# Optimization experiments

Measured on AMD Instinct MI355X. Metric: run time of the kernel, lower is better.

## Reference

```python
import jax, jax.numpy as jnp
import numpy as np

NUM_HEADS = 16
EMBED_DIM = 2048
MAX_SEQ = 2048
HEAD_SIZE = EMBED_DIM // NUM_HEADS  # 128
ROPE_BASE = 10000.0


def setup_inputs() -> dict:
    key = jax.random.key(0)
    k1, k2, k3 = jax.random.split(key, 3)
    B, S = 4, 2048
    x = jax.random.normal(k1, (B, S, EMBED_DIM), dtype=jnp.float32)
    positions = jnp.arange(S, dtype=jnp.int32)
    # causal boolean mask: query i may attend to key j iff j <= i
    mask = jnp.tril(jnp.ones((S, MAX_SEQ), dtype=bool))[None, None]
    Wqkv = jax.random.normal(k2, (EMBED_DIM, 3 * EMBED_DIM), dtype=jnp.float32) * 0.02
    Wout = jax.random.normal(k3, (EMBED_DIM, EMBED_DIM), dtype=jnp.float32) * 0.02
    return {"x": x, "positions": positions, "mask": mask, "Wqkv": Wqkv, "Wout": Wout}


def _rope(x, positions):
    # x: [B, S, H, hd]; rotate interleaved (even, odd) pairs in last dim
    inv_freq = 1.0 / (ROPE_BASE ** (jnp.arange(0, HEAD_SIZE, 2, dtype=jnp.float32) / HEAD_SIZE))
    freq = positions.astype(jnp.float32)[:, None] * inv_freq[None, :]  # [S, hd/2]
    cos = jnp.cos(freq)[None, :, None, :]  # [1, S, 1, hd/2]
    sin = jnp.sin(freq)[None, :, None, :]
    xp = x.reshape(*x.shape[:-1], HEAD_SIZE // 2, 2)
    x0, x1 = xp[..., 0], xp[..., 1]
    out = jnp.stack([x0 * cos - x1 * sin, x1 * cos + x0 * sin], axis=-1)
    return out.reshape(x.shape)


def reference(x, positions, mask, Wqkv, Wout):
    B, S, D = x.shape
    H, hd = NUM_HEADS, HEAD_SIZE
    qkv = x @ Wqkv  # [B, S, 3D]
    q, k, v = jnp.split(qkv, 3, axis=-1)
    q = q.reshape(B, S, H, hd)
    k = k.reshape(B, S, H, hd)
    v = v.reshape(B, S, H, hd)
    q = _rope(q, positions)
    k = _rope(k, positions)
    # [B, H, S, hd]
    q = q.transpose(0, 2, 1, 3)
    k = k.transpose(0, 2, 1, 3)
    v = v.transpose(0, 2, 1, 3)
    # KV-cache update: write k/v at `positions` into a zero-initialized cache
    cache_k = jnp.zeros((B, H, MAX_SEQ, hd), dtype=x.dtype)
    cache_v = jnp.zeros((B, H, MAX_SEQ, hd), dtype=x.dtype)
    k = cache_k.at[:, :, positions].set(k)
    v = cache_v.at[:, :, positions].set(v)
    scale = 1.0 / jnp.sqrt(jnp.float32(hd))
    scores = jnp.einsum('bhqd,bhkd->bhqk', q, k) * scale  # [B, H, S, MAX_SEQ]
    scores = jnp.where(mask, scores, jnp.float32(-1e30))
    attn = jax.nn.softmax(scores, axis=-1)
    y = jnp.einsum('bhqk,bhkd->bhqd', attn, v)  # [B, H, S, hd]
    y = y.transpose(0, 2, 1, 3).reshape(B, S, D)
    return y @ Wout
```

## Files before the change

### kernel.cpp

```cpp
#include <hip/hip_runtime.h>
#include <hip/hip_bf16.h>
#include <cstdint>
#include <cstddef>

constexpr int CS = 2048;
constexpr int CHD = 128;
constexpr int CD = 2048;
constexpr int CN3 = 6144;

typedef __attribute__((ext_vector_type(8))) short short8;
typedef __attribute__((ext_vector_type(4))) float f32x4;
typedef __attribute__((ext_vector_type(4))) int int4v;

#define GLOAD_LDS16(g, l) __builtin_amdgcn_global_load_lds( \
    (const __attribute__((address_space(1))) void*)(g),      \
    (__attribute__((address_space(3))) void*)(l), 16, 0, 0)

__device__ __forceinline__ unsigned short f2bf(float f) {
  union { float f; unsigned u; } v; v.f = f;
  unsigned r = v.u + 0x7fffu + ((v.u >> 16) & 1u);
  return (unsigned short)(r >> 16);
}
__device__ __forceinline__ unsigned pkbf(float a, float b) {
  return (unsigned)f2bf(a) | ((unsigned)f2bf(b) << 16);
}

__device__ __forceinline__ float dpp_xor1(float x) {
  return __builtin_bit_cast(float, __builtin_amdgcn_update_dpp(
      __builtin_bit_cast(int, x), __builtin_bit_cast(int, x), 0xB1, 0xf, 0xf, true));
}

__global__ __launch_bounds__(256) void k_cvt(const float* __restrict__ in,
                                             unsigned short* __restrict__ out, int n) {
  int i = (blockIdx.x * 256 + threadIdx.x) * 8;
  if (i >= n) return;
  float4 a = *(const float4*)(in + i);
  float4 b = *(const float4*)(in + i + 4);
  short8 o;
  o[0] = (short)f2bf(a.x); o[1] = (short)f2bf(a.y);
  o[2] = (short)f2bf(a.z); o[3] = (short)f2bf(a.w);
  o[4] = (short)f2bf(b.x); o[5] = (short)f2bf(b.y);
  o[6] = (short)f2bf(b.z); o[7] = (short)f2bf(b.w);
  *(short8*)(out + i) = o;
}

__global__ __launch_bounds__(256) void k_transcvt(const float* __restrict__ in,
                                                  unsigned short* __restrict__ out,
                                                  int R, int C) {
  __shared__ float tile[32][33];
  int c0 = blockIdx.x * 32, r0 = blockIdx.y * 32;
  int tx = threadIdx.x & 31, ty = threadIdx.x >> 5;
#pragma unroll
  for (int j = 0; j < 4; ++j)
    tile[ty + 8 * j][tx] = in[(size_t)(r0 + ty + 8 * j) * C + c0 + tx];
  __syncthreads();
#pragma unroll
  for (int j = 0; j < 4; ++j)
    out[(size_t)(c0 + ty + 8 * j) * R + r0 + tx] = f2bf(tile[tx][ty + 8 * j]);
}

__global__ void k_ropetab(float2* __restrict__ tab) {
  int p = blockIdx.x, c = threadIdx.x;
  float inv = powf(10000.0f, -(float)(2 * c) / 128.0f);
  float a = (float)p * inv;
  tab[p * 64 + c] = make_float2(cosf(a), sinf(a));
}

__global__ __launch_bounds__(512, 2) void k_gemm32(
    const unsigned short* __restrict__ A,
    const unsigned short* __restrict__ Bt,
    unsigned short* __restrict__ outQ,
    unsigned short* __restrict__ outK,
    unsigned short* __restrict__ outV,
    const int* __restrict__ positions,
    const float2* __restrict__ tab,
    int K, int nbn) {
  const int nwg = gridDim.x;
  const int cpx = nwg >> 3;
  const int wg = blockIdx.x;
  const int swz = (wg & 7) * cpx + (wg >> 3);
  const int bn = swz % nbn, bm = swz / nbn;

  const int t = threadIdx.x;
  const int w = t >> 6, lane = t & 63;
  const int wr = w >> 2, wc = w & 3;
  const int lr = lane & 15, lg = lane >> 4;

  __shared__ char L[65536];

  const size_t Kb = (size_t)K * 2;
  const int srow = t >> 2;
  const int sslot = ((t & 3) ^ ((t >> 3) & 3)) * 16;
  const char* gA = (const char*)A + (size_t)(bm * 256 + srow) * Kb + sslot;
  const char* gB = (const char*)Bt + (size_t)(bn * 256 + srow) * Kb + sslot;

#define STG(BUFB, OP, J, KT)                                                   \
  GLOAD_LDS16(((OP) ? gB : gA) + (size_t)((J) * 128) * Kb + (size_t)(KT) * 64, \
              L + (BUFB) + (OP) * 16384 + (J) * 8192 + t * 16)

  const int xo2 = (lr >> 1) & 3;
  const int aR = (wr * 128 + lr) * 64;
  const int bR = (wc * 64 + lr) * 64;
#define RA(BUFB, MI) (*(const short8*)(L + (BUFB) + aR + (MI) * 1024 + ((lg ^ xo2) << 4)))
#define RB(BUFB, NI) (*(const short8*)(L + (BUFB) + 16384 + bR + (NI) * 1024 + ((lg ^ xo2) << 4)))

  f32x4 acc[8][4] = {};
  const int ktiles = K >> 5;

  STG(0, 0, 0, 0); STG(0, 0, 1, 0); STG(0, 1, 0, 0); STG(0, 1, 1, 0);
  STG(32768, 0, 0, 1);
  asm volatile("s_waitcnt vmcnt(1)" ::: "memory");
  __builtin_amdgcn_s_barrier();

  short8 af[4], bf[4];
  int c = 0;
  for (int kt = 0; kt < ktiles - 1; ++kt) {
    const int cb = c << 15, nb = (c ^ 1) << 15;
#pragma unroll
    for (int mi = 0; mi < 4; ++mi) af[mi] = RA(cb, mi);
#pragma unroll
    for (int ni = 0; ni < 2; ++ni) bf[ni] = RB(cb, ni);
    STG(nb, 0, 1, kt + 1);
    __builtin_amdgcn_s_setprio(1);
#pragma unroll
    for (int mi = 0; mi < 4; ++mi)
#pragma unroll
      for (int ni = 0; ni < 2; ++ni)
        acc[mi][ni] = __builtin_amdgcn_mfma_f32_16x16x32_bf16(af[mi], bf[ni], acc[mi][ni], 0, 0, 0);
    __builtin_amdgcn_s_setprio(0);
#pragma unroll
    for (int ni = 2; ni < 4; ++ni) bf[ni] = RB(cb, ni);
    STG(nb, 1, 0, kt + 1);
    __builtin_amdgcn_s_setprio(1);
#pragma unroll
    for (int mi = 0; mi < 4; ++mi)
#pragma unroll
      for (int ni = 2; ni < 4; ++ni)
        acc[mi][ni] = __builtin_amdgcn_mfma_f32_16x16x32_bf16(af[mi], bf[ni], acc[mi][ni], 0, 0, 0);
    __builtin_amdgcn_s_setprio(0);
#pragma unroll
    for (int mi = 0; mi < 4; ++mi) af[mi] = RA(cb, mi + 4);
    STG(nb, 1, 1, kt + 1);
    __builtin_amdgcn_s_setprio(1);
#pragma unroll
    for (int mi = 0; mi < 4; ++mi)
#pragma unroll
      for (int ni = 2; ni < 4; ++ni)
        acc[mi + 4][ni] = __builtin_amdgcn_mfma_f32_16x16x32_bf16(af[mi], bf[ni], acc[mi + 4][ni], 0, 0, 0);
    __builtin_amdgcn_s_setprio(0);
    __builtin_amdgcn_s_setprio(1);
#pragma unroll
    for (int mi = 0; mi < 4; ++mi)
#pragma unroll
      for (int ni = 0; ni < 2; ++ni)
        acc[mi + 4][ni] = __builtin_amdgcn_mfma_f32_16x16x32_bf16(af[mi], bf[ni], acc[mi + 4][ni], 0, 0, 0);
    __builtin_amdgcn_s_setprio(0);

    __builtin_amdgcn_s_barrier();
    if (kt + 2 < ktiles) {
      STG(cb, 0, 0, kt + 2);
      asm volatile("s_waitcnt vmcnt(1)" ::: "memory");
    } else {
      asm volatile("s_waitcnt vmcnt(0)" ::: "memory");
    }
    __builtin_amdgcn_s_barrier();
    c ^= 1;
  }
  {
    const int cb = c << 15;
#pragma unroll
    for (int mi = 0; mi < 4; ++mi) af[mi] = RA(cb, mi);
#pragma unroll
    for (int ni = 0; ni < 2; ++ni) bf[ni] = RB(cb, ni);
    __builtin_amdgcn_s_setprio(1);
#pragma unroll
    for (int mi = 0; mi < 4; ++mi)
#pragma unroll
      for (int ni = 0; ni < 2; ++ni)
        acc[mi][ni] = __builtin_amdgcn_mfma_f32_16x16x32_bf16(af[mi], bf[ni], acc[mi][ni], 0, 0, 0);
    __builtin_amdgcn_s_setprio(0);
#pragma unroll
    for (int ni = 2; ni < 4; ++ni) bf[ni] = RB(cb, ni);
    __builtin_amdgcn_s_setprio(1);
#pragma unroll
    for (int mi = 0; mi < 4; ++mi)
#pragma unroll
      for (int ni = 2; ni < 4; ++ni)
        acc[mi][ni] = __builtin_amdgcn_mfma_f32_16x16x32_bf16(af[mi], bf[ni], acc[mi][ni], 0, 0, 0);
    __builtin_amdgcn_s_setprio(0);
#pragma unroll
    for (int mi = 0; mi < 4; ++mi) af[mi] = RA(cb, mi + 4);
    __builtin_amdgcn_s_setprio(1);
#pragma unroll
    for (int mi = 0; mi < 4; ++mi)
#pragma unroll
      for (int ni = 0; ni < 4; ++ni)
        acc[mi + 4][ni] = __builtin_amdgcn_mfma_f32_16x16x32_bf16(af[mi], bf[ni], acc[mi + 4][ni], 0, 0, 0);
    __builtin_amdgcn_s_setprio(0);
  }
#undef STG
#undef RA
#undef RB

  const int which = bn >> 3;
  if (which < 2) {
    const float qsc = which ? 1.0f : 0.08838834764831845f;
    unsigned short* dstB = which ? outK : outQ;
#pragma unroll
    for (int mi = 0; mi < 8; ++mi)
#pragma unroll
      for (int rr = 0; rr < 4; ++rr) {
        int mg = bm * 256 + wr * 128 + mi * 16 + lg * 4 + rr;
        int bb = mg >> 11, s = mg & 2047;
        int pos = positions[s];
        int srow2 = which ? pos : s;
        const float2* tb = tab + pos * 64 + wc * 32 + (lr >> 1);
#pragma unroll
        for (int ni = 0; ni < 4; ++ni) {
          int cn = bn * 256 + wc * 64 + ni * 16 + lr;
          int h = (cn >> 7) & 15, d = cn & 127;
          float x = acc[mi][ni][rr];
          float p = dpp_xor1(x);
          float2 cs = tb[ni * 8];
          float y = (lr & 1) ? (x * cs.x + p * cs.y)
                             : (x * cs.x - p * cs.y);
          dstB[((size_t)(bb * 16 + h) * CS + srow2) * CHD + d] = f2bf(y * qsc);
        }
      }
  } else {
    unsigned short* TL = (unsigned short*)L;
    const int bb = bm >> 3, s0 = (bm & 7) * 256;
    const int h0 = bn * 2 - 32;
    const int vcr = t >> 1, hs = t & 1;
    unsigned short* vrow = outV +
        ((size_t)((bb * 16 + h0 + (vcr >> 7)) * 128 + (vcr & 127))) * CS + s0;
#pragma unroll
    for (int hh = 0; hh < 2; ++hh) {
      __syncthreads();
      if (wr == hh) {
#pragma unroll
        for (int mi = 0; mi < 8; ++mi) {
          int sb = mi * 16 + lg * 4;
#pragma unroll
          for (int ni = 0; ni < 4; ++ni) {
            int vc = wc * 64 + ni * 16 + lr;
            unsigned lo = pkbf(acc[mi][ni][0], acc[mi][ni][1]);
            unsigned hi2 = pkbf(acc[mi][ni][2], acc[mi][ni][3]);
            unsigned long long v8 = (unsigned long long)lo | ((unsigned long long)hi2 << 32);
            *(unsigned long long*)(TL + vc * 128 + (sb ^ ((vc & 7) << 3))) = v8;
          }
        }
      }
      __syncthreads();
#pragma unroll
      for (int j = 0; j < 8; ++j) {
        short8 v = *(const short8*)(TL + vcr * 128 + ((hs * 64 + j * 8) ^ ((vcr & 7) << 3)));
        *(short8*)(vrow + hh * 128 + hs * 64 + j * 8) = v;
      }
    }
  }
}

template <int EPI>
__global__ __launch_bounds__(512, 2) void k_gemm256(
    const unsigned short* __restrict__ A,
    const unsigned short* __restrict__ Bt,
    float* __restrict__ outF,
    int M, int N, int K, int nbn) {
  const int nwg = gridDim.x;
  const int cpx = nwg >> 3;
  const int wg = blockIdx.x;
  const int swz = (wg & 7) * cpx + (wg >> 3);
  const int bn = swz % nbn, bm = swz / nbn;

  const int t = threadIdx.x;
  const int w = t >> 6, lane = t & 63;
  const int wr = w >> 2, wc = w & 3;
  const int lr = lane & 15, lg = lane >> 4;

  __shared__ char L[131072];

  const size_t Kb = (size_t)K * 2;
  const int srl = w * 16 + (lane >> 3);
  const int sch = ((lane & 7) ^ (lane >> 3)) * 16;
  const char* gA = (const char*)A + (size_t)(bm * 256 + srl) * Kb + sch;
  const char* gB = (const char*)Bt + (size_t)(bn * 256 + srl) * Kb + sch;
  const int ldst = w * 2048 + lane * 16;

#define STAGE(BUFB, OP, HALF, J, KT)                                               \
  GLOAD_LDS16(((OP) ? gB : gA) + (size_t)((HALF) * 128 + (J) * 8) * Kb +           \
                  (size_t)(KT) * 128,                                              \
              L + (BUFB) + (OP) * 32768 + (HALF) * 16384 + (J) * 1024 + ldst)

  const int xo = lr & 7;
  const int aRow = (wr * 128 + lr) * 128;
  const int bRow = (wc * 64 + lr) * 128;
#define RDA(BUFB, MI, KH) \
  (*(const short8*)(L + (BUFB) + aRow + (MI) * 2048 + ((((KH) * 4 + lg) ^ xo) << 4)))
#define RDB(BUFB, NI, KH) \
  (*(const short8*)(L + (BUFB) + 32768 + bRow + (NI) * 2048 + ((((KH) * 4 + lg) ^ xo) << 4)))

  f32x4 acc[8][4] = {};
  const int ktiles = K >> 6;

#pragma unroll
  for (int h = 0; h < 2; ++h)
#pragma unroll
    for (int j = 0; j < 2; ++j) { STAGE(0, 0, h, j, 0); STAGE(0, 1, h, j, 0); }
  if (ktiles > 1) {
    STAGE(65536, 0, 0, 0, 1); STAGE(65536, 0, 0, 1, 1);
    asm volatile("s_waitcnt vmcnt(2)" ::: "memory");
  } else {
    asm volatile("s_waitcnt vmcnt(0)" ::: "memory");
  }
  __builtin_amdgcn_s_barrier();

  short8 afr[4][2], bfr[4][2];

#define KTILE_PHASES(CB, NB, KT, DOSTAGE)                                          \
                                              \
  _Pragma("unroll") for (int mi = 0; mi < 4; ++mi)                                 \
      _Pragma("unroll") for (int kh = 0; kh < 2; ++kh)                             \
          afr[mi][kh] = RDA(CB, mi, kh);                                           \
  _Pragma("unroll") for (int ni = 0; ni < 2; ++ni)                                 \
      _Pragma("unroll") for (int kh = 0; kh < 2; ++kh)                             \
          bfr[ni][kh] = RDB(CB, ni, kh);                                           \
  if (DOSTAGE) { STAGE(NB, 0, 1, 0, (KT) + 1); STAGE(NB, 0, 1, 1, (KT) + 1); }     \
  __builtin_amdgcn_s_setprio(1);                                                   \
  _Pragma("unroll") for (int mi = 0; mi < 4; ++mi)                                 \
      _Pragma("unroll") for (int ni = 0; ni < 2; ++ni)                             \
          _Pragma("unroll") for (int kh = 0; kh < 2; ++kh)                         \
              acc[mi][ni] = __builtin_amdgcn_mfma_f32_16x16x32_bf16(               \
                  afr[mi][kh], bfr[ni][kh], acc[mi][ni], 0, 0, 0);                 \
  __builtin_amdgcn_s_setprio(0);                                                   \
                                                     \
  _Pragma("unroll") for (int ni = 2; ni < 4; ++ni)                                 \
      _Pragma("unroll") for (int kh = 0; kh < 2; ++kh)                             \
          bfr[ni][kh] = RDB(CB, ni, kh);                                           \
  if (DOSTAGE) { STAGE(NB, 1, 0, 0, (KT) + 1); STAGE(NB, 1, 0, 1, (KT) + 1); }     \
  __builtin_amdgcn_s_setprio(1);                                                   \
  _Pragma("unroll") for (int mi = 0; mi < 4; ++mi)                                 \
      _Pragma("unroll") for (int ni = 2; ni < 4; ++ni)                             \
          _Pragma("unroll") for (int kh = 0; kh < 2; ++kh)                         \
              acc[mi][ni] = __builtin_amdgcn_mfma_f32_16x16x32_bf16(               \
                  afr[mi][kh], bfr[ni][kh], acc[mi][ni], 0, 0, 0);                 \
  __builtin_amdgcn_s_setprio(0);                                                   \
                                                    \
  _Pragma("unroll") for (int mi = 0; mi < 4; ++mi)                                 \
      _Pragma("unroll") for (int kh = 0; kh < 2; ++kh)                             \
          afr[mi][kh] = RDA(CB, mi + 4, kh);                                       \
  if (DOSTAGE) { STAGE(NB, 1, 1, 0, (KT) + 1); STAGE(NB, 1, 1, 1, (KT) + 1); }     \
  __builtin_amdgcn_s_setprio(1);                                                   \
  _Pragma("unroll") for (int mi = 0; mi < 4; ++mi)                                 \
      _Pragma("unroll") for (int ni = 2; ni < 4; ++ni)                             \
          _Pragma("unroll") for (int kh = 0; kh < 2; ++kh)                         \
              acc[mi + 4][ni] = __builtin_amdgcn_mfma_f32_16x16x32_bf16(           \
                  afr[mi][kh], bfr[ni][kh], acc[mi + 4][ni], 0, 0, 0);             \
  __builtin_amdgcn_s_setprio(0);                                                   \
                                                       \
  __builtin_amdgcn_s_setprio(1);                                                   \
  _Pragma("unroll") for (int mi = 0; mi < 4; ++mi)                                 \
      _Pragma("unroll") for (int ni = 0; ni < 2; ++ni)                             \
          _Pragma("unroll") for (int kh = 0; kh < 2; ++kh)                         \
              acc[mi + 4][ni] = __builtin_amdgcn_mfma_f32_16x16x32_bf16(           \
                  afr[mi][kh], bfr[ni][kh], acc[mi + 4][ni], 0, 0, 0);             \
  __builtin_amdgcn_s_setprio(0);

  int c = 0;
  for (int kt = 0; kt < ktiles - 1; ++kt) {
    const int cb = c << 16, nb = (c ^ 1) << 16;
    KTILE_PHASES(cb, nb, kt, true)
    __builtin_amdgcn_s_barrier();
    if (kt + 2 < ktiles) {
      STAGE(cb, 0, 0, 0, kt + 2); STAGE(cb, 0, 0, 1, kt + 2);
      asm volatile("s_waitcnt vmcnt(2)" ::: "memory");
    } else {
      asm volatile("s_waitcnt vmcnt(0)" ::: "memory");
    }
    __builtin_amdgcn_s_barrier();
    c ^= 1;
  }
  {
    const int cb = c << 16, nb = 0;
    KTILE_PHASES(cb, nb, 0, false)
  }
#undef KTILE_PHASES
#undef STAGE
#undef RDA
#undef RDB

#pragma unroll
  for (int mi = 0; mi < 8; ++mi)
#pragma unroll
    for (int rr = 0; rr < 4; ++rr) {
      int mg = bm * 256 + wr * 128 + mi * 16 + lg * 4 + rr;
#pragma unroll
      for (int ni = 0; ni < 4; ++ni)
        outF[(size_t)mg * N + bn * 256 + wc * 64 + ni * 16 + lr] = acc[mi][ni][rr];
    }
}

__global__ __launch_bounds__(256, 3) void k_attn(
    const unsigned short* __restrict__ Q,
    const unsigned short* __restrict__ Kc,
    const unsigned short* __restrict__ Vt,
    unsigned short* __restrict__ Y) {
  const int qt_h = 15 - (blockIdx.x >> 6);
  const int bh = blockIdx.x & 63;
  const int q0 = qt_h * 128;
  const int t = threadIdx.x;
  const int w = t >> 6, lane = t & 63;
  const int lr = lane & 15, lg = lane >> 4;
  const int b = bh >> 4, h = bh & 15;

  __shared__ unsigned short lK[3][32 * 128];
  __shared__ unsigned short lVt[3][128 * 32];

  const char* kg = (const char*)(Kc + (size_t)bh * CS * CHD);
  const char* vtg = (const char*)(Vt + (size_t)bh * CHD * CS);

  short8 qf[2][4];
#pragma unroll
  for (int qt = 0; qt < 2; ++qt)
#pragma unroll
    for (int ks = 0; ks < 4; ++ks)
      qf[qt][ks] = *(const short8*)(Q + ((size_t)bh * CS + q0 + w * 32 + qt * 16 + lr) * CHD + ks * 32 + lg * 8);

  f32x4 accy[2][8] = {};
  f32x4 accl[2] = {};
  float m[2] = {-1e30f, -1e30f};

  short8 vone;
  {
    short o16 = (lr == 0) ? (short)0x3F80 : (short)0;
#pragma unroll
    for (int e = 0; e < 8; ++e) vone[e] = o16;
  }

  const int nch = 4 * qt_h + 4;
  const int qmaxw = q0 + w * 32 + 31;

  auto stage = [&](int ch, int buf) {
    const int kv0 = ch * 32;
    char* dK = (char*)lK[buf];
    char* dV = (char*)lVt[buf];
#pragma unroll
    for (int i = 0; i < 2; ++i) {
      int kr = w * 8 + i * 4 + lg;
      GLOAD_LDS16(kg + (size_t)(kv0 + kr) * 256 + ((lr * 16) ^ ((kr & 7) << 4)),
                  dK + w * 2048 + i * 1024 + lane * 16);
    }
#pragma unroll
    for (int i = 0; i < 2; ++i) {
      int vd = w * 32 + i * 16 + (lane >> 2);
      GLOAD_LDS16(vtg + (size_t)vd * 4096 + (size_t)kv0 * 2 + (lane & 3) * 16,
                  dV + w * 2048 + i * 1024 + lane * 16);
    }
  };

  stage(0, 0);
  stage(1, 1);
  int cur = 0, nxt = 2;
  for (int ch = 0; ch < nch; ++ch) {
    if (ch + 1 < nch) {
      asm volatile("s_waitcnt vmcnt(4)" ::: "memory");
    } else {
      asm volatile("s_waitcnt vmcnt(0)" ::: "memory");
    }
    __builtin_amdgcn_s_barrier();
    if (ch + 2 < nch) stage(ch + 2, nxt);

    const int kv0 = ch * 32;
    const unsigned short* bK = lK[cur];
    const unsigned short* bV = lVt[cur];
    cur = cur == 2 ? 0 : cur + 1;
    nxt = nxt == 2 ? 0 : nxt + 1;

    if (kv0 <= qmaxw) {
      f32x4 sv[2][2] = {};
#pragma unroll
      for (int kvt = 0; kvt < 2; ++kvt) {
        short8 kf[4];
#pragma unroll
        for (int ks = 0; ks < 4; ++ks) {
          int row = kvt * 16 + lr;
          kf[ks] = *(const short8*)((const char*)bK + row * 256 + ((ks * 64 + lg * 16) ^ ((row & 7) << 4)));
        }
#pragma unroll
        for (int qt = 0; qt < 2; ++qt)
#pragma unroll
          for (int ks = 0; ks < 4; ++ks)
            sv[qt][kvt] = __builtin_amdgcn_mfma_f32_16x16x32_bf16(kf[ks], qf[qt][ks], sv[qt][kvt], 0, 0, 0);
      }

      float p8[2][8];
      float pm[2];
      bool need = false;
#pragma unroll
      for (int qt = 0; qt < 2; ++qt) {
        const int qi = q0 + w * 32 + qt * 16 + lr;
        float mx = -1e30f;
#pragma unroll
        for (int kvt = 0; kvt < 2; ++kvt)
#pragma unroll
          for (int r = 0; r < 4; ++r) {
            int kv = kv0 + kvt * 16 + lg * 4 + r;
            float s = (kv <= qi) ? sv[qt][kvt][r] : -1e30f;
            p8[qt][kvt * 4 + r] = s;
            mx = fmaxf(mx, s);
          }
        mx = fmaxf(mx, __shfl_xor(mx, 32, 64));
        mx = fmaxf(mx, __shfl_xor(mx, 16, 64));
        pm[qt] = mx;
        need = need || (mx > m[qt] + 8.0f);
      }

      if (__any((int)need)) {
#pragma unroll
        for (int qt = 0; qt < 2; ++qt) {
          float nm = fmaxf(m[qt], pm[qt]);
          float fr = __expf(m[qt] - nm);
          m[qt] = nm;
#pragma unroll
          for (int r = 0; r < 4; ++r) {
            int idx = (((lane >> 4) << 2) + r) << 2;
            float frT = __builtin_bit_cast(float,
                __builtin_amdgcn_ds_bpermute(idx, __builtin_bit_cast(int, fr)));
#pragma unroll
            for (int dt = 0; dt < 8; ++dt) accy[qt][dt][r] *= frT;
            accl[qt][r] *= frT;
          }
        }
      }

      short8 pa[2];
      const int sA = lr + ((lane & 16) << 1);
      const int sB = sA + 16;
      const bool hi = (lane >= 32);
#pragma unroll
      for (int qt = 0; qt < 2; ++qt) {
        float pe0 = __expf(p8[qt][0] - m[qt]);
        float pe1 = __expf(p8[qt][1] - m[qt]);
        float pe2 = __expf(p8[qt][2] - m[qt]);
        float pe3 = __expf(p8[qt][3] - m[qt]);
        float pe4 = __expf(p8[qt][4] - m[qt]);
        float pe5 = __expf(p8[qt][5] - m[qt]);
        float pe6 = __expf(p8[qt][6] - m[qt]);
        float pe7 = __expf(p8[qt][7] - m[qt]);
        unsigned w0 = pkbf(pe0, pe1);
        unsigned w1 = pkbf(pe2, pe3);
        unsigned w2 = pkbf(pe4, pe5);
        unsigned w3 = pkbf(pe6, pe7);
        unsigned a0 = (unsigned)__shfl((int)w0, sA, 64);
        unsigned a2 = (unsigned)__shfl((int)w2, sA, 64);
        unsigned b0 = (unsigned)__shfl((int)w1, sA, 64);
        unsigned b2 = (unsigned)__shfl((int)w3, sA, 64);
        unsigned c0 = (unsigned)__shfl((int)w0, sB, 64);
        unsigned c2 = (unsigned)__shfl((int)w2, sB, 64);
        unsigned d0 = (unsigned)__shfl((int)w1, sB, 64);
        unsigned d2 = (unsigned)__shfl((int)w3, sB, 64);
        int4v xi;
        xi[0] = (int)(hi ? a2 : a0);
        xi[1] = (int)(hi ? b2 : b0);
        xi[2] = (int)(hi ? c2 : c0);
        xi[3] = (int)(hi ? d2 : d0);
        pa[qt] = __builtin_bit_cast(short8, xi);
      }

#pragma unroll
      for (int dt = 0; dt < 8; ++dt) {
        short8 vf = *(const short8*)((const char*)bV + (dt * 16 + lr) * 64 + lg * 16);
#pragma unroll
        for (int qt = 0; qt < 2; ++qt)
          accy[qt][dt] = __builtin_amdgcn_mfma_f32_16x16x32_bf16(pa[qt], vf, accy[qt][dt], 0, 0, 0);
      }
#pragma unroll
      for (int qt = 0; qt < 2; ++qt)
        accl[qt] = __builtin_amdgcn_mfma_f32_16x16x32_bf16(pa[qt], vone, accl[qt], 0, 0, 0);
    }
  }

#pragma unroll
  for (int qt = 0; qt < 2; ++qt)
#pragma unroll
    for (int r = 0; r < 4; ++r) {
      float lsum = accl[qt][r];
      lsum = __shfl(lsum, lane & 48, 64);
      float inv = 1.0f / lsum;
      int qrow = q0 + w * 32 + qt * 16 + lg * 4 + r;
      unsigned short* yr = Y + ((size_t)(b * CS + qrow)) * CD + h * CHD;
#pragma unroll
      for (int dt = 0; dt < 8; ++dt)
        yr[dt * 16 + lr] = f2bf(accy[qt][dt][r] * inv);
    }
}

extern "C" void kernel_launch(void* const* d_in, const int* in_sizes, int n_in,
                              void* d_out, int out_size, void* d_ws, size_t ws_size,
                              hipStream_t stream) {
  const float* x = (const float*)d_in[0];
  const int* positions = (const int*)d_in[1];
  const float* Wqkv = (const float*)d_in[3];
  const float* Wout = (const float*)d_in[4];
  float* out = (float*)d_out;

  char* ws = (char*)d_ws;
  size_t off = 0;
  auto alloc = [&](size_t bytes) {
    char* p = ws + off;
    off += (bytes + 255) & ~(size_t)255;
    return p;
  };
  unsigned short* q_bf = (unsigned short*)alloc((size_t)64 * CS * CHD * 2);
  unsigned short* k_bf = (unsigned short*)alloc((size_t)64 * CS * CHD * 2);
  unsigned short* v_bf = (unsigned short*)alloc((size_t)64 * CS * CHD * 2);
  unsigned short* xw = (unsigned short*)alloc((size_t)8192 * CD * 2);
  unsigned short* wT = (unsigned short*)alloc((size_t)CN3 * CD * 2);
  float2* tab = (float2*)alloc((size_t)CS * 64 * sizeof(float2));


  k_cvt<<<8192, 256, 0, stream>>>(x, xw, 8192 * CD);
  k_transcvt<<<dim3(CN3 / 32, CD / 32), 256, 0, stream>>>(Wqkv, wT, CD, CN3);
  k_ropetab<<<CS, 64, 0, stream>>>(tab);
  k_gemm32<<<768, 512, 0, stream>>>(xw, wT, q_bf, k_bf, v_bf,
                                    positions, tab, CD, 24);
  k_transcvt<<<dim3(CD / 32, CD / 32), 256, 0, stream>>>(Wout, wT, CD, CD);
  k_attn<<<1024, 256, 0, stream>>>(q_bf, k_bf, v_bf, xw);
  k_gemm256<1><<<256, 512, 0, stream>>>(xw, wT, out, 8192, CD, CD, 8);
}
```

Measured before the change: 424.8 us.

## Shrink QKV GEMM tile to 256x128 and use XCD-grouped block mapping

The QKV projection GEMM now uses 256-thread blocks computing 256x128 output tiles over 1536 workgroups, instead of 512-thread blocks with 256x256 tiles over 768 workgroups. The LDS staging, double-buffer offsets and the Q/K/V epilogue indexing are adjusted to match. Both GEMMs get a new block-to-tile mapping that groups neighbouring M/N tiles onto the same XCD for better L2 reuse. The aim is better wave balance across CUs and higher occupancy from the smaller LDS footprint. The cost is lower arithmetic reuse per tile and more re-reads of the A matrix.

```diff
diff --git a/kernel.cpp b/kernel.cpp
--- a/kernel.cpp
+++ b/kernel.cpp
@@ -66,7 +66,7 @@
   tab[p * 64 + c] = make_float2(cosf(a), sinf(a));
 }
 
-__global__ __launch_bounds__(512, 2) void k_gemm32(
+__global__ __launch_bounds__(256, 2) void k_gemm1(
     const unsigned short* __restrict__ A,
     const unsigned short* __restrict__ Bt,
     unsigned short* __restrict__ outQ,
@@ -74,29 +74,28 @@
     unsigned short* __restrict__ outV,
     const int* __restrict__ positions,
     const float2* __restrict__ tab,
-    int K, int nbn) {
-  const int nwg = gridDim.x;
-  const int cpx = nwg >> 3;
+    int K) {
   const int wg = blockIdx.x;
-  const int swz = (wg & 7) * cpx + (wg >> 3);
-  const int bn = swz % nbn, bm = swz / nbn;
+  const int l = wg >> 3;
+  const int bm = (wg & 7) * 4 + ((l >> 4) & 3);
+  const int bn = (l >> 6) * 16 + (l & 15);
 
   const int t = threadIdx.x;
   const int w = t >> 6, lane = t & 63;
-  const int wr = w >> 2, wc = w & 3;
+  const int wr = w >> 1, wc = w & 1;
   const int lr = lane & 15, lg = lane >> 4;
 
-  __shared__ char L[65536];
+  __shared__ char L[49152];
 
   const size_t Kb = (size_t)K * 2;
   const int srow = t >> 2;
   const int sslot = ((t & 3) ^ ((t >> 3) & 3)) * 16;
   const char* gA = (const char*)A + (size_t)(bm * 256 + srow) * Kb + sslot;
-  const char* gB = (const char*)Bt + (size_t)(bn * 256 + srow) * Kb + sslot;
+  const char* gB = (const char*)Bt + (size_t)(bn * 128 + srow) * Kb + sslot;
 
 #define STG(BUFB, OP, J, KT)                                                   \
-  GLOAD_LDS16(((OP) ? gB : gA) + (size_t)((J) * 128) * Kb + (size_t)(KT) * 64, \
-              L + (BUFB) + (OP) * 16384 + (J) * 8192 + t * 16)
+  GLOAD_LDS16(((OP) ? gB : gA) + (size_t)((J) * 64) * Kb + (size_t)(KT) * 64,  \
+              L + (BUFB) + (OP) * 16384 + (J) * 4096 + t * 16)
 
   const int xo2 = (lr >> 1) & 3;
   const int aR = (wr * 128 + lr) * 64;
@@ -107,20 +106,21 @@
   f32x4 acc[8][4] = {};
   const int ktiles = K >> 5;
 
-  STG(0, 0, 0, 0); STG(0, 0, 1, 0); STG(0, 1, 0, 0); STG(0, 1, 1, 0);
-  STG(32768, 0, 0, 1);
+  STG(0, 0, 0, 0); STG(0, 0, 1, 0); STG(0, 0, 2, 0); STG(0, 0, 3, 0);
+  STG(0, 1, 0, 0); STG(0, 1, 1, 0);
+  STG(24576, 0, 0, 1);
   asm volatile("s_waitcnt vmcnt(1)" ::: "memory");
   __builtin_amdgcn_s_barrier();
 
   short8 af[4], bf[4];
   int c = 0;
   for (int kt = 0; kt < ktiles - 1; ++kt) {
-    const int cb = c << 15, nb = (c ^ 1) << 15;
+    const int cb = c * 24576, nb = (c ^ 1) * 24576;
 #pragma unroll
     for (int mi = 0; mi < 4; ++mi) af[mi] = RA(cb, mi);
 #pragma unroll
     for (int ni = 0; ni < 2; ++ni) bf[ni] = RB(cb, ni);
-    STG(nb, 0, 1, kt + 1);
+    STG(nb, 0, 1, kt + 1); STG(nb, 0, 2, kt + 1);
     __builtin_amdgcn_s_setprio(1);
 #pragma unroll
     for (int mi = 0; mi < 4; ++mi)
@@ -130,7 +130,7 @@
     __builtin_amdgcn_s_setprio(0);
 #pragma unroll
     for (int ni = 2; ni < 4; ++ni) bf[ni] = RB(cb, ni);
-    STG(nb, 1, 0, kt + 1);
+    STG(nb, 0, 3, kt + 1); STG(nb, 1, 0, kt + 1);
     __builtin_amdgcn_s_setprio(1);
 #pragma unroll
     for (int mi = 0; mi < 4; ++mi)
@@ -167,7 +167,7 @@
     c ^= 1;
   }
   {
-    const int cb = c << 15;
+    const int cb = c * 24576;
 #pragma unroll
     for (int mi = 0; mi < 4; ++mi) af[mi] = RA(cb, mi);
 #pragma unroll
@@ -202,7 +202,7 @@
 #undef RA
 #undef RB
 
-  const int which = bn >> 3;
+  const int which = bn >> 4;
   if (which < 2) {
     const float qsc = which ? 1.0f : 0.08838834764831845f;
     unsigned short* dstB = which ? outK : outQ;
@@ -217,7 +217,7 @@
         const float2* tb = tab + pos * 64 + wc * 32 + (lr >> 1);
 #pragma unroll
         for (int ni = 0; ni < 4; ++ni) {
-          int cn = bn * 256 + wc * 64 + ni * 16 + lr;
+          int cn = bn * 128 + wc * 64 + ni * 16 + lr;
           int h = (cn >> 7) & 15, d = cn & 127;
           float x = acc[mi][ni][rr];
           float p = dpp_xor1(x);
@@ -229,11 +229,10 @@
       }
   } else {
     unsigned short* TL = (unsigned short*)L;
+    const int h0 = bn & 15;
     const int bb = bm >> 3, s0 = (bm & 7) * 256;
-    const int h0 = bn * 2 - 32;
-    const int vcr = t >> 1, hs = t & 1;
-    unsigned short* vrow = outV +
-        ((size_t)((bb * 16 + h0 + (vcr >> 7)) * 128 + (vcr & 127))) * CS + s0;
+    const int row = t >> 1, hs = t & 1;
+    unsigned short* vrow = outV + ((size_t)((bb * 16 + h0) * 128 + row)) * CS + s0;
 #pragma unroll
     for (int hh = 0; hh < 2; ++hh) {
       __syncthreads();
@@ -254,7 +253,7 @@
       __syncthreads();
 #pragma unroll
       for (int j = 0; j < 8; ++j) {
-        short8 v = *(const short8*)(TL + vcr * 128 + ((hs * 64 + j * 8) ^ ((vcr & 7) << 3)));
+        short8 v = *(const short8*)(TL + row * 128 + ((hs * 64 + j * 8) ^ ((row & 7) << 3)));
         *(short8*)(vrow + hh * 128 + hs * 64 + j * 8) = v;
       }
     }
@@ -267,11 +266,11 @@
     const unsigned short* __restrict__ Bt,
     float* __restrict__ outF,
     int M, int N, int K, int nbn) {
-  const int nwg = gridDim.x;
-  const int cpx = nwg >> 3;
+  (void)nbn;
   const int wg = blockIdx.x;
-  const int swz = (wg & 7) * cpx + (wg >> 3);
-  const int bn = swz % nbn, bm = swz / nbn;
+  const int l = wg >> 3;
+  const int bm = (wg & 7) * 4 + ((l >> 3) & 3);
+  const int bn = (l >> 5) * 8 + (l & 7);
 
   const int t = threadIdx.x;
   const int w = t >> 6, lane = t & 63;
@@ -622,8 +621,7 @@
   k_cvt<<<8192, 256, 0, stream>>>(x, xw, 8192 * CD);
   k_transcvt<<<dim3(CN3 / 32, CD / 32), 256, 0, stream>>>(Wqkv, wT, CD, CN3);
   k_ropetab<<<CS, 64, 0, stream>>>(tab);
-  k_gemm32<<<768, 512, 0, stream>>>(xw, wT, q_bf, k_bf, v_bf,
-                                    positions, tab, CD, 24);
+  k_gemm1<<<1536, 256, 0, stream>>>(xw, wT, q_bf, k_bf, v_bf, positions, tab, CD);
   k_transcvt<<<dim3(CD / 32, CD / 32), 256, 0, stream>>>(Wout, wT, CD, CD);
   k_attn<<<1024, 256, 0, stream>>>(q_bf, k_bf, v_bf, xw);
   k_gemm256<1><<<256, 512, 0, stream>>>(xw, wT, out, 8192, CD, CD, 8);
```

Result: no change. 425.3 us (+0.1%).
